# Kernel optimization log

Hardware: AMD Instinct MI355X
Metric: run time of the kernel (lower is better)

Reference implementation:

```python
import jax, jax.numpy as jnp
import numpy as np
import math

RADIUS = 1.0
PERCENTAGES = (0.02, 0.04, 0.06, 0.08, 0.10)


def _fps(pts, npoint):
    """Furthest point sampling. pts: [N,3] -> idx [npoint] int32 (starts at index 0,
    matching pointnet2 CUDA furthest_point_sample)."""
    N = pts.shape[0]

    def step(carry, _):
        dists, last = carry
        d = jnp.sum((pts - pts[last]) ** 2, axis=-1)
        dists = jnp.minimum(dists, d)
        nxt = jnp.argmax(dists).astype(jnp.int32)
        return (dists, nxt), nxt

    init = (jnp.full((N,), 1e10, pts.dtype), jnp.int32(0))
    _, rest = jax.lax.scan(step, init, None, length=npoint - 1)
    return jnp.concatenate([jnp.zeros((1,), jnp.int32), rest])


def _ball_query(pcd, queries, r, nsample):
    """pcd [B,N,3], queries [B,M,3] -> idx [B,M,nsample] int32.
    First (by index order) points with squared dist < r^2; groups with fewer than
    nsample in-radius points are padded with the first found index (pn2 semantics)."""
    N = pcd.shape[1]
    d2 = jnp.sum((queries[:, :, None, :] - pcd[:, None, :, :]) ** 2, axis=-1)  # [B,M,N]
    key = jnp.where(d2 < r * r, jnp.arange(N, dtype=jnp.int32), jnp.int32(N))
    srt = jnp.sort(key, axis=-1)[:, :, :nsample]  # first in-radius indices
    valid = srt < N
    first = jnp.where(srt[:, :, :1] < N, srt[:, :, :1], 0)
    return jnp.where(valid, srt, first)


def _nn_dist(g):
    """g [G,n,3] -> [G,n] distance to nearest neighbor (2nd-smallest pairwise
    Euclidean distance, i.e. KNN(k=2) dist[:,:,1] including self-distance 0)."""
    sq = jnp.sum(g * g, axis=-1)  # [G,n]
    d2 = sq[:, :, None] + sq[:, None, :] - 2.0 * jnp.einsum('gnc,gmc->gnm', g, g)
    d2 = jnp.maximum(d2, 0.0)
    # safe sqrt (zero grad at exact zeros: self / duplicated padded points)
    d = jnp.where(d2 > 0, jnp.sqrt(jnp.where(d2 > 0, d2, 1.0)), 0.0)
    neg2, _ = jax.lax.top_k(-d, 2)  # two smallest distances
    return -neg2[:, :, 1]


def _uniform_loss(pcd):
    B, N, C = pcd.shape
    npoint = int(N * 0.05)
    fps_idx = jax.vmap(_fps, in_axes=(0, None))(pcd, npoint)  # [B,M]
    new_xyz = jnp.take_along_axis(pcd, fps_idx[:, :, None], axis=1)  # [B,M,3]
    loss = jnp.zeros((), pcd.dtype)
    for p in PERCENTAGES:
        nsample = int(N * p)
        r = math.sqrt(p * RADIUS)
        disk_area = math.pi * RADIUS ** 2 / N
        expect_len = math.sqrt(disk_area)
        idx = _ball_query(pcd, new_xyz, r, nsample)  # [B,M,n]
        grouped = jax.vmap(lambda pts, ii: pts[ii])(pcd, idx)  # [B,M,n,3]
        g = grouped.reshape(B * npoint, nsample, C)
        nn = _nn_dist(g)  # [G,n]
        e_ = 0.1
        u = jnp.abs(nn + e_)
        u = jnp.mean(u, axis=1)  # [G]
        u = (u - expect_len) ** 2 / (expect_len + e_)
        loss = loss + jnp.mean(u) * (p * 100.0) ** 2
    return loss / len(PERCENTAGES)


def setup_inputs() -> dict:
    key = jax.random.key(0)
    pcd = jax.random.uniform(key, (2, 4096, 3), dtype=jnp.float32)
    return {"pcd": pcd}


def reference(pcd):
    return _uniform_loss(pcd)
```

## Files before the change

kernel.cpp:

```cpp
#include <hip/hip_runtime.h>
#include <cmath>

#define NPTS 4096
#define NPOINT 204
#define NPCT 5
#define MAXNS 409
#define FPS_T 256
#define NGROUP 408
#define NPART (NGROUP * NPCT)
#define MAXSLOT 7

#define NBLOCKS 512
#define NWORKER 510
#define NROUND  4

#define SMEM_BYTES 65600
#define KEYS_OFF   65536
#define WRES_OFF   6544
#define WTOT_OFF   20880
#define SPART_OFF  20896
#define SCTL_OFF   20912

typedef unsigned long long u64;
typedef float f32x2 __attribute__((ext_vector_type(2)));

struct LossParams {
    int   nsample[NPCT];
    float r2[NPCT];
    float wscale[NPCT];
    float expect_len;
};

__device__ int g_fps[NGROUP];
__device__ int g_done;

template <int CTRL>
__device__ __forceinline__ int dpp_imax(int v) {
    int t = __builtin_amdgcn_update_dpp(0, v, CTRL, 0xf, 0xf, true);
    return v > t ? v : t;
}
template <int CTRL>
__device__ __forceinline__ int dpp_imin(int v) {
    int t = __builtin_amdgcn_update_dpp(0x7fffffff, v, CTRL, 0xf, 0xf, false);
    return v < t ? v : t;
}
__device__ __forceinline__ int wave_max_i(int v) {
    v = dpp_imax<0x111>(v); v = dpp_imax<0x112>(v);
    v = dpp_imax<0x114>(v); v = dpp_imax<0x118>(v);
    v = dpp_imax<0x142>(v); v = dpp_imax<0x143>(v);
    return __builtin_amdgcn_readlane(v, 63);
}
__device__ __forceinline__ int wave_min_i(int v) {
    v = dpp_imin<0x111>(v); v = dpp_imin<0x112>(v);
    v = dpp_imin<0x114>(v); v = dpp_imin<0x118>(v);
    v = dpp_imin<0x142>(v); v = dpp_imin<0x143>(v);
    return __builtin_amdgcn_readlane(v, 63);
}
template <int CTRL>
__device__ __forceinline__ u64 dpp_u64max(u64 v) {
    int lo = (int)(unsigned)v;
    int hi = (int)(unsigned)(v >> 32);
    unsigned slo = (unsigned)__builtin_amdgcn_update_dpp(0, lo, CTRL, 0xf, 0xf, true);
    unsigned shi = (unsigned)__builtin_amdgcn_update_dpp(0, hi, CTRL, 0xf, 0xf, true);
    u64 o = ((u64)shi << 32) | slo;
    return v > o ? v : o;
}

__device__ void fps_role(const float* __restrict__ pcd, char* smem) {
#pragma clang fp contract(off)
    __builtin_amdgcn_s_setprio(3);
    float4* pts = reinterpret_cast<float4*>(smem);
    u64 (*keys)[4] = reinterpret_cast<u64 (*)[4]>(smem + KEYS_OFF);

    const int b = blockIdx.x;
    const int t = threadIdx.x;
    const int wave = t >> 6, lane = t & 63;
    const float* base = pcd + (size_t)b * NPTS * 3;

    f32x2 X[8], Y[8], Z[8], D[8];
    #pragma unroll
    for (int q = 0; q < 8; ++q) {
        int n0 = (2 * q) * FPS_T + t;
        int n1 = (2 * q + 1) * FPS_T + t;
        float x0 = base[3 * n0 + 0], y0 = base[3 * n0 + 1], z0 = base[3 * n0 + 2];
        float x1 = base[3 * n1 + 0], y1 = base[3 * n1 + 1], z1 = base[3 * n1 + 2];
        pts[n0] = make_float4(x0, y0, z0, 0.0f);
        pts[n1] = make_float4(x1, y1, z1, 0.0f);
        X[q] = (f32x2){x0, x1};
        Y[q] = (f32x2){y0, y1};
        Z[q] = (f32x2){z0, z1};
        D[q] = (f32x2){1e10f, 1e10f};
    }
    int* out = g_fps + b * NPOINT;
    if (t == 0)
        __hip_atomic_store(&out[0], ~0, __ATOMIC_RELAXED, __HIP_MEMORY_SCOPE_AGENT);
    __syncthreads();

    float4 c = pts[0];
    for (int it = 1; it < NPOINT; ++it) {
        f32x2 cxx = (f32x2){c.x, c.x};
        f32x2 cyy = (f32x2){c.y, c.y};
        f32x2 czz = (f32x2){c.z, c.z};
        int tb[8], ti[8];
        #pragma unroll
        for (int q = 0; q < 8; ++q) {
            f32x2 dx = X[q] - cxx, dy = Y[q] - cyy, dz = Z[q] - czz;
            f32x2 d  = (dx * dx + dy * dy) + dz * dz;
            f32x2 dd = D[q];
            float d0 = fminf(dd.x, d.x);
            float d1 = fminf(dd.y, d.y);
            D[q] = (f32x2){d0, d1};
            int b0 = __float_as_int(d0);
            int b1 = __float_as_int(d1);
            bool c0 = b0 >= b1;
            tb[q] = c0 ? b0 : b1;
            ti[q] = c0 ? (2 * q) * FPS_T + t : (2 * q + 1) * FPS_T + t;
        }
        #pragma unroll
        for (int st = 1; st < 8; st <<= 1) {
            #pragma unroll
            for (int q = 0; q < 8; q += 2 * st) {
                bool cc = tb[q] >= tb[q + st];
                tb[q] = cc ? tb[q] : tb[q + st];
                ti[q] = cc ? ti[q] : ti[q + st];
            }
        }
        int bb = tb[0], bi = ti[0];

        int wmax = wave_max_i(bb);
        int cand = (bb == wmax) ? bi : 0x7fffffff;
        int widx = wave_min_i(cand);
        if (lane == 0)
            keys[it & 1][wave] =
                ((u64)(unsigned)wmax << 32) | (unsigned)~(unsigned)widx;
        __syncthreads();
        u64 kv = keys[it & 1][lane & 3];
        kv = dpp_u64max<0x111>(kv);
        kv = dpp_u64max<0x112>(kv);
        unsigned lo3 = (unsigned)__builtin_amdgcn_readlane((int)(unsigned)kv, 3);
        int last = (int)~lo3;
        c = pts[last];
        if (t == 0)
            __hip_atomic_store(&out[it], ~last, __ATOMIC_RELAXED, __HIP_MEMORY_SCOPE_AGENT);
    }
}

template <int K>
__device__ __forceinline__ void phaseB(const float4* __restrict__ gpts,
                                       float2 (*wres)[64],
                                       int j0, int j1, int lane, int cntB) {
    float4 pi[K];
    float m1[K], m2[K];
    #pragma unroll
    for (int s = 0; s < K; ++s) {
        int idx = s * 64 + lane;
        pi[s] = gpts[idx < cntB ? idx : 0];
        m1[s] = 1e30f; m2[s] = 1e30f;
    }
    #pragma unroll 2
    for (int j = j0; j < j1; ++j) {
        float4 a = gpts[j];
        #pragma unroll
        for (int s = 0; s < K; ++s) {
            float tt = pi[s].x * a.x;
            tt = fmaf(pi[s].y, a.y, tt);
            tt = fmaf(pi[s].z, a.z, tt);
            float h = fmaf(-2.0f, tt, a.w);
            m2[s] = __builtin_amdgcn_fmed3f(m1[s], m2[s], h);
            m1[s] = fminf(m1[s], h);
        }
    }
    #pragma unroll
    for (int s = 0; s < K; ++s) wres[s][lane] = (float2){m1[s], m2[s]};
}

__device__ void worker_role(const float* __restrict__ pcd,
                            float* __restrict__ partials,
                            float* __restrict__ out,
                            const LossParams& P, char* smem) {
    float4* gpts = reinterpret_cast<float4*>(smem);
    auto wres    = reinterpret_cast<float2 (*)[MAXSLOT][64]>(smem + WRES_OFF);
    int*   s_wtot = reinterpret_cast<int*>(smem + WTOT_OFF);
    float* s_part = reinterpret_cast<float*>(smem + SPART_OFF);
    int*   s_ctl  = reinterpret_cast<int*>(smem + SCTL_OFF);

    const int w = blockIdx.x - 2;
    const int t = threadIdx.x;
    const int wave = t >> 6, lane = t & 63;

    for (int round = 0; round < NROUND; ++round) {
        const int tau  = w + round * NWORKER;
        const int m_   = tau / 10;
        const int rem  = tau - m_ * 10;
        const int b    = rem / 5;
        const int pidx = rem - b * 5;

        const int   ns = P.nsample[pidx];
        const float r2 = P.r2[pidx];
        const float* base = pcd + (size_t)b * NPTS * 3;

        if (t == 0) {
            int v;
            while ((v = __hip_atomic_load(&g_fps[b * NPOINT + m_],
                                          __ATOMIC_RELAXED,
                                          __HIP_MEMORY_SCOPE_AGENT)) >= 0)
                __builtin_amdgcn_s_sleep(16);
            s_ctl[0] = ~v;
        }
        __syncthreads();
        const int qi = s_ctl[0];
        float qx = base[3 * qi + 0], qy = base[3 * qi + 1], qz = base[3 * qi + 2];

        unsigned long long msk[16];
        int lbase[16];
        int run = 0;
        #pragma unroll 4
        for (int s = 0; s < 16; ++s) {
            int n = wave * 1024 + s * 64 + lane;
            float x = base[3 * n + 0];
            float y = base[3 * n + 1];
            float z = base[3 * n + 2];
            float d2;
            {
#pragma clang fp contract(off)
                float dx = qx - x, dy = qy - y, dz = qz - z;
                float aa = dx * dx, bb2 = dy * dy, cc = dz * dz;
                d2 = (aa + bb2) + cc;
            }
            msk[s] = __ballot(d2 < r2);
            lbase[s] = run;
            run += __popcll(msk[s]);
        }
        if (lane == 0) s_wtot[wave] = run;
        __syncthreads();
        int w0 = s_wtot[0], w1 = s_wtot[1], w2 = s_wtot[2], w3 = s_wtot[3];
        int Bw = (wave > 0 ? w0 : 0) + (wave > 1 ? w1 : 0) + (wave > 2 ? w2 : 0);
        int cnt  = w0 + w1 + w2 + w3;
        int cntB = cnt < ns ? cnt : ns;
        const int npad = ns - cntB;

        #pragma unroll 4
        for (int s = 0; s < 16; ++s) {
            int gb = Bw + lbase[s];
            if (gb >= ns) break;
            unsigned long long mk = msk[s];
            bool in = (mk >> lane) & 1ull;
            int pos = gb + __popcll(mk & ((1ull << lane) - 1ull));
            if (in && pos < ns) {
                int n = wave * 1024 + s * 64 + lane;
                float x = base[3 * n], y = base[3 * n + 1], z = base[3 * n + 2];
                float sq = fmaf(x, x, fmaf(y, y, z * z));
                gpts[pos] = make_float4(x, y, z, sq);
            }
        }
        __syncthreads();

        const int quarter = (cntB + 3) >> 2;
        const int j0 = wave * quarter;
        const int j1 = (j0 + quarter) < cntB ? (j0 + quarter) : cntB;
        const int nslot = (cntB + 63) >> 6;
        switch (nslot) {
            case 1: phaseB<1>(gpts, wres[wave], j0, j1, lane, cntB); break;
            case 2: phaseB<2>(gpts, wres[wave], j0, j1, lane, cntB); break;
            case 3: phaseB<3>(gpts, wres[wave], j0, j1, lane, cntB); break;
            case 4: phaseB<4>(gpts, wres[wave], j0, j1, lane, cntB); break;
            case 5: phaseB<5>(gpts, wres[wave], j0, j1, lane, cntB); break;
            case 6: phaseB<6>(gpts, wres[wave], j0, j1, lane, cntB); break;
            default: phaseB<7>(gpts, wres[wave], j0, j1, lane, cntB); break;
        }
        __syncthreads();

        float sum = 0.0f;
        for (int it = t; it < nslot * 64; it += 256) {
            int i = it;
            if (i < cntB) {
                int s = it >> 6, l = it & 63;
                float2 a  = wres[0][s][l];
                float2 bq = wres[1][s][l];
                float2 cq = wres[2][s][l];
                float2 dq = wres[3][s][l];
                float e1 = fminf(a.x, bq.x), e2 = fminf(fmaxf(a.x, bq.x), fminf(a.y, bq.y));
                float f1 = fminf(cq.x, dq.x), f2 = fminf(fmaxf(cq.x, dq.x), fminf(cq.y, dq.y));
                float m2v = fminf(fmaxf(e1, f1), fminf(e2, f2));
                float sq = gpts[i].w;
                float d2 = fmaxf(sq + m2v, 0.0f);
                if (!(i == 0 && npad > 0)) sum += sqrtf(d2);
            }
        }
        #pragma unroll
        for (int off = 32; off; off >>= 1) sum += __shfl_down(sum, off);
        if (lane == 0) s_part[wave] = sum;
        __syncthreads();
        if (t == 0) {
            float tot = s_part[0] + s_part[1] + s_part[2] + s_part[3] + 0.1f * (float)ns;
            float u  = tot / (float)ns;
            float du = u - P.expect_len;
            partials[tau] = du * du / (P.expect_len + 0.1f) * P.wscale[pidx];
        }
    }

    if (t == 0) {
        int old = __hip_atomic_fetch_add(&g_done, 1, __ATOMIC_ACQ_REL,
                                         __HIP_MEMORY_SCOPE_AGENT);
        s_ctl[0] = old;
    }
    __syncthreads();
    if (s_ctl[0] == NWORKER - 1) {
        (void)__hip_atomic_load(&g_done, __ATOMIC_ACQUIRE, __HIP_MEMORY_SCOPE_AGENT);
        float s = 0.0f;
        for (int i = t; i < NPART; i += 256) s += partials[i];
        #pragma unroll
        for (int off = 32; off; off >>= 1) s += __shfl_down(s, off);
        if (lane == 0) s_part[wave] = s;
        __syncthreads();
        if (t == 0) out[0] = s_part[0] + s_part[1] + s_part[2] + s_part[3];
        for (int i = t; i < NGROUP; i += 256) g_fps[i] = 0;
        if (t == 0) g_done = 0;
    }
}

__global__ __launch_bounds__(256, 2) void fused_kernel(const float* __restrict__ pcd,
                                                       float* __restrict__ partials,
                                                       float* __restrict__ out,
                                                       LossParams P) {
    __shared__ __align__(16) char smem[SMEM_BYTES];
    if (blockIdx.x < 2) {
        fps_role(pcd, smem);
    } else {
        worker_role(pcd, partials, out, P, smem);
    }
}

extern "C" void kernel_launch(void* const* d_in, const int* in_sizes, int n_in,
                              void* d_out, int out_size, void* d_ws, size_t ws_size,
                              hipStream_t stream) {
    const float* pcd = (const float*)d_in[0];
    float* out = (float*)d_out;
    float* partials = (float*)d_ws;

    LossParams P;
    const double ps[NPCT] = {0.02, 0.04, 0.06, 0.08, 0.10};
    for (int i = 0; i < NPCT; ++i) {
        P.nsample[i] = (int)(NPTS * ps[i]);
        double r = std::sqrt(ps[i] * 1.0);
        P.r2[i] = (float)(r * r);
        double w = (ps[i] * 100.0) * (ps[i] * 100.0);
        P.wscale[i] = (float)(w / (double)(2 * NPOINT * NPCT));
    }
    P.expect_len = (float)std::sqrt(3.14159265358979323846 / (double)NPTS);

    fused_kernel<<<dim3(NBLOCKS), dim3(256), 0, stream>>>(pcd, partials, out, P);
}
```

Baseline: 194.9 us.

## Idle blocks sharing CUs with FPS and simplify per-thread argmax

```diff
diff --git a/kernel.cpp b/kernel.cpp
--- a/kernel.cpp
+++ b/kernel.cpp
@@ -11,7 +11,7 @@
 #define MAXSLOT 7
 
 #define NBLOCKS 512
-#define NWORKER 510
+#define NWORKER 508
 #define NROUND  4
 
 #define SMEM_BYTES 65600
@@ -101,7 +101,7 @@
         f32x2 cxx = (f32x2){c.x, c.x};
         f32x2 cyy = (f32x2){c.y, c.y};
         f32x2 czz = (f32x2){c.z, c.z};
-        int tb[8], ti[8];
+        int bb = -1, bi = 0;
         #pragma unroll
         for (int q = 0; q < 8; ++q) {
             f32x2 dx = X[q] - cxx, dy = Y[q] - cyy, dz = Z[q] - czz;
@@ -112,21 +112,9 @@
             D[q] = (f32x2){d0, d1};
             int b0 = __float_as_int(d0);
             int b1 = __float_as_int(d1);
-            bool c0 = b0 >= b1;
-            tb[q] = c0 ? b0 : b1;
-            ti[q] = c0 ? (2 * q) * FPS_T + t : (2 * q + 1) * FPS_T + t;
-        }
-        #pragma unroll
-        for (int st = 1; st < 8; st <<= 1) {
-            #pragma unroll
-            for (int q = 0; q < 8; q += 2 * st) {
-                bool cc = tb[q] >= tb[q + st];
-                tb[q] = cc ? tb[q] : tb[q + st];
-                ti[q] = cc ? ti[q] : ti[q + st];
-            }
-        }
-        int bb = tb[0], bi = ti[0];
-
+            if (b0 > bb) { bb = b0; bi = (2 * q) * FPS_T + t; }
+            if (b1 > bb) { bb = b1; bi = (2 * q + 1) * FPS_T + t; }
+        }
         int wmax = wave_max_i(bb);
         int cand = (bb == wmax) ? bi : 0x7fffffff;
         int widx = wave_min_i(cand);
@@ -177,19 +165,18 @@
 __device__ void worker_role(const float* __restrict__ pcd,
                             float* __restrict__ partials,
                             float* __restrict__ out,
-                            const LossParams& P, char* smem) {
+                            const LossParams& P, char* smem, int w) {
     float4* gpts = reinterpret_cast<float4*>(smem);
     auto wres    = reinterpret_cast<float2 (*)[MAXSLOT][64]>(smem + WRES_OFF);
     int*   s_wtot = reinterpret_cast<int*>(smem + WTOT_OFF);
     float* s_part = reinterpret_cast<float*>(smem + SPART_OFF);
     int*   s_ctl  = reinterpret_cast<int*>(smem + SCTL_OFF);
 
-    const int w = blockIdx.x - 2;
     const int t = threadIdx.x;
     const int wave = t >> 6, lane = t & 63;
 
-    for (int round = 0; round < NROUND; ++round) {
-        const int tau  = w + round * NWORKER;
+    for (int round = (w < 8 ? -1 : 0); round < NROUND; ++round) {
+        const int tau  = (round < 0) ? w : 8 + w + round * NWORKER;
         const int m_   = tau / 10;
         const int rem  = tau - m_ * 10;
         const int b    = rem / 5;
@@ -297,6 +284,7 @@
             float du = u - P.expect_len;
             partials[tau] = du * du / (P.expect_len + 0.1f) * P.wscale[pidx];
         }
+        __syncthreads();
     }
 
     if (t == 0) {
@@ -324,10 +312,13 @@
                                                        float* __restrict__ out,
                                                        LossParams P) {
     __shared__ __align__(16) char smem[SMEM_BYTES];
-    if (blockIdx.x < 2) {
+    const int bid = blockIdx.x;
+    if (bid == 256 || bid == 257) return;
+    if (bid < 2) {
         fps_role(pcd, smem);
     } else {
-        worker_role(pcd, partials, out, P, smem);
+        const int w = (bid < 256) ? bid - 2 : bid - 4;
+        worker_role(pcd, partials, out, P, smem, w);
     }
 }
 
```

Measured after the change: 193.6 us. Within noise of the previous version (-0.7%).
